# Kernel tuning notes

Hardware: AMD Instinct MI355X
Metric: run time of the kernel (lower is better)

Reference implementation:

```python
import jax, jax.numpy as jnp
import numpy as np

N_ATOMS = 5000
N_PAIRS = 160000
N_STRUCT = 16
N_SPECIES = 4
L_MAX = 2
K = 128            # k_max per l (rectangular)
N_BASIS = 8        # radial basis size
RAD_HIDDEN = 32    # radial MLP hidden
CUTOFF = 5.0
MSG_SCALE = 0.1767767   # ~1/sqrt(avg_degree)
INIT_SCALE = 0.2        # hypers['initial_scaling']


def _orthogonal(key, n):
    m = jax.random.normal(key, (n, n))
    q, r = jnp.linalg.qr(m)
    return q * jnp.sign(jnp.diag(r))[None, :]


def setup_inputs() -> dict:
    key = jax.random.key(0)
    ks = jax.random.split(key, 24)
    positions = jax.random.normal(ks[0], (N_ATOMS, 3)) * 1.5
    cells = jax.random.normal(ks[1], (N_STRUCT, 3, 3)) * 0.5
    species = jax.random.randint(ks[2], (N_ATOMS,), 0, N_SPECIES)
    cell_shifts = jax.random.randint(ks[3], (N_PAIRS, 3), 0, 3).astype(jnp.int32)
    center_indices = jax.random.randint(ks[4], (N_PAIRS,), 0, N_ATOMS)
    neighbor_indices = jax.random.randint(ks[5], (N_PAIRS,), 0, N_ATOMS)
    structure_pairs = jax.random.randint(ks[6], (N_PAIRS,), 0, N_STRUCT)
    s = lambda k, sh, f: jax.random.normal(k, sh) * f
    params = dict(
        embed=s(ks[7], (N_SPECIES, K), 1.0),
        rad_w1=s(ks[8], (N_BASIS, RAD_HIDDEN), 0.3), rad_b1=jnp.zeros((RAD_HIDDEN,)),
        rad_w2=s(ks[9], (RAD_HIDDEN, (L_MAX + 1) * K), 0.3), rad_b2=jnp.zeros(((L_MAX + 1) * K,)),
        erad_w1=s(ks[10], (N_BASIS, RAD_HIDDEN), 0.3), erad_b1=jnp.zeros((RAD_HIDDEN,)),
        erad_w2=s(ks[11], (RAD_HIDDEN, (L_MAX + 1) * K), 0.3), erad_b2=jnp.zeros(((L_MAX + 1) * K,)),
        mix_a=s(ks[12], (L_MAX + 1, K), 0.5),
        emix_a=s(ks[13], (L_MAX + 1, K), 0.5),
        head_w1=s(ks[14], (K, K), 0.1), head_b1=jnp.zeros((K,)),
        head_w2=s(ks[15], (K, K), 0.1), head_b2=jnp.zeros((K,)),
        last_w=s(ks[16], (K, 1), 0.1), last_b=jnp.zeros((1,)),
        U2=_orthogonal(ks[20], 9),  # orthogonal CG change-of-basis, U @ U.T = I
    )
    return dict(positions=positions, cells=cells, species=species,
                cell_shifts=cell_shifts, center_indices=center_indices,
                neighbor_indices=neighbor_indices, structure_pairs=structure_pairs,
                **params)


def _sph(unit):
    # real spherical harmonics up to l=2, inputs are unit vectors [P,3]
    x, y, z = unit[:, 0], unit[:, 1], unit[:, 2]
    sh0 = jnp.ones_like(x)[:, None]
    sh1 = jnp.stack([y, z, x], axis=1)
    c = jnp.sqrt(3.0)
    sh2 = jnp.stack([c * x * y, c * y * z, 0.5 * (3 * z * z - 1.0),
                     c * x * z, 0.5 * c * (x * x - y * y)], axis=1)
    return [sh0, sh1, sh2]


def _radial(d, w1, b1, w2, b2):
    # Gaussian radial basis * smooth cutoff -> MLP -> per-l K channels
    centers = jnp.linspace(0.0, CUTOFF, N_BASIS)
    rb = jnp.exp(-((d[:, None] - centers[None, :]) ** 2) / (2.0 * 0.5 ** 2))
    fcut = jnp.where(d < CUTOFF, 0.5 * (jnp.cos(jnp.pi * d / CUTOFF) + 1.0), 0.0)
    h = jax.nn.silu((rb * fcut[:, None]) @ w1 + b1)
    return (h @ w2 + b2).reshape(-1, L_MAX + 1, K)  # [P, l, K]


def _uncouple(f, l, U2):
    # coupled [N, 2l+1, K] -> uncoupled matrix [N, 3, 3, K] (padded_l = 2)
    if l == 0:
        return f[:, :, None, :]
    n, _, k = f.shape
    vec = jnp.zeros((n, 9, k), f.dtype)
    off = 1 if l == 1 else 4
    vec = vec.at[:, off:off + 2 * l + 1, :].set(f)
    unc = jnp.einsum('qp,nqk->npk', U2, vec)  # U2.T @ vec
    return unc.reshape(n, 3, 3, k)


def _couple(unc, l, U2):
    if l == 0:
        return unc[:, :, 0, :]
    n, k = unc.shape[0], unc.shape[-1]
    vec = jnp.einsum('pq,nqk->npk', U2, unc.reshape(n, 9, k))
    off = 1 if l == 1 else 4
    return vec[:, off:off + 2 * l + 1, :]


def _cg_iterate(feats, U2, mix):
    # CG tensor product iteration in the uncoupled (matrix) basis:
    # matrix product A@A is equivariant under A -> D A D^T
    out = []
    for l, f in enumerate(feats):
        A = _uncouple(f, l, U2)
        C = jnp.einsum('nimk,nmjk->nijk', A, A)
        out.append(_couple(A + C * mix[l][None, None, None, :], l, U2))
    return out


def _forward(positions, cells, embed, rad_w1, rad_b1, rad_w2, rad_b2,
             erad_w1, erad_b1, erad_w2, erad_b2, mix_a, emix_a,
             head_w1, head_b1, head_w2, head_b2, last_w, last_b, U2,
             species, cell_shifts, center_indices, neighbor_indices, structure_pairs):
    # pair vectors with PBC shifts
    shifts = cell_shifts.astype(positions.dtype) - 1.0  # -> {-1,0,1}
    vec = positions[neighbor_indices] - positions[center_indices] \
        + jnp.einsum('pi,pij->pj', shifts, cells[structure_pairs])
    d = jnp.sqrt(jnp.sum(vec * vec, axis=1) + 1e-12)
    unit = vec / d[:, None]
    sh = [s * INIT_SCALE for s in _sph(unit)]
    Rk = _radial(d, rad_w1, rad_b1, rad_w2, rad_b2)      # [P, 3, K]
    emb_n = embed[species][neighbor_indices]             # [P, K]

    # invariant message passing: sh_l x radial x neighbor embedding, scatter to centers
    feats = []
    for l in range(L_MAX + 1):
        msg = sh[l][:, :, None] * Rk[:, l, None, :] * emb_n[:, None, :]
        feats.append(jax.ops.segment_sum(msg, center_indices, num_segments=N_ATOMS) * MSG_SCALE)

    feats = _cg_iterate(feats, U2, mix_a)

    # equivariant message passing layer
    Rke = _radial(d, erad_w1, erad_b1, erad_w2, erad_b2)
    inv_n = feats[0][neighbor_indices, 0, :]             # [P, K] invariant part
    new = []
    for l in range(L_MAX + 1):
        g = feats[l][neighbor_indices]                   # [P, 2l+1, K]
        msg = sh[l][:, :, None] * Rke[:, l, None, :] * inv_n[:, None, :] \
            + Rke[:, 0, None, :] * g
        new.append(feats[l] + jax.ops.segment_sum(msg, center_indices, num_segments=N_ATOMS) * MSG_SCALE)

    feats = _cg_iterate(new, U2, emix_a)

    # scalar (l=0) MLP head + last linear layer
    h = feats[0][:, 0, :]
    h = jax.nn.silu(h @ head_w1 + head_b1)
    h = jax.nn.silu(h @ head_w2 + head_b2)
    return h @ last_w + last_b  # [N_ATOMS, 1]


def reference(positions, cells, species, cell_shifts, center_indices,
              neighbor_indices, structure_pairs, embed, rad_w1, rad_b1, rad_w2,
              rad_b2, erad_w1, erad_b1, erad_w2, erad_b2, mix_a, emix_a,
              head_w1, head_b1, head_w2, head_b2, last_w, last_b, U2):
    return _forward(positions, cells, embed, rad_w1, rad_b1, rad_w2, rad_b2,
                    erad_w1, erad_b1, erad_w2, erad_b2, mix_a, emix_a,
                    head_w1, head_b1, head_w2, head_b2, last_w, last_b, U2,
                    species, cell_shifts, center_indices, neighbor_indices,
                    structure_pairs)
```

## Files before the change

### kernel.cpp

```cpp
#include <hip/hip_runtime.h>

constexpr int   kAtoms  = 5000;
constexpr int   kPairs  = 160000;
constexpr int   KD      = 128;
constexpr int   NB      = 8;
constexpr int   RH      = 32;
constexpr float kCutoff = 5.0f;
constexpr float kPi     = 3.14159265358979323846f;
constexpr float C1 = 0.2f * 0.1767767f;
constexpr float C2 = 1.2f * 0.1767767f;
constexpr int   CHUNK = 96;

__device__ __forceinline__ float silu(float x) { return x / (1.0f + __expf(-x)); }


__global__ __launch_bounds__(256) void hist_kernel(
    const int* __restrict__ ctr, int* __restrict__ cnt)
{
    int p = blockIdx.x * 256 + threadIdx.x;
    atomicAdd(cnt + ctr[p], 1);
}

__global__ __launch_bounds__(1024) void scan_kernel(
    const int* __restrict__ cnt, int* __restrict__ off, int* __restrict__ cur)
{
    __shared__ int s_part[1024];
    const int CH = 5;
    int t = threadIdx.x;
    int base = t * CH;
    int loc[CH];
    int run = 0;
    #pragma unroll
    for (int i = 0; i < CH; i++) {
        int idx = base + i;
        int v = (idx < kAtoms) ? cnt[idx] : 0;
        loc[i] = run;
        run += v;
    }
    s_part[t] = run;
    __syncthreads();
    for (int st = 1; st < 1024; st <<= 1) {
        int v = (t >= st) ? s_part[t - st] : 0;
        __syncthreads();
        s_part[t] += v;
        __syncthreads();
    }
    int excl = (t > 0) ? s_part[t - 1] : 0;
    #pragma unroll
    for (int i = 0; i < CH; i++) {
        int idx = base + i;
        if (idx < kAtoms) { off[idx] = excl + loc[i]; cur[idx] = excl + loc[i]; }
    }
    if (t == 1023) off[kAtoms] = s_part[1023];
}

__global__ __launch_bounds__(256) void build_kernel(
    const float* __restrict__ pos, const float* __restrict__ cells,
    const int* __restrict__ species, const int* __restrict__ shifts,
    const int* __restrict__ ctr, const int* __restrict__ nbr,
    const int* __restrict__ spair,
    int* __restrict__ cur, int* __restrict__ nbrs_s, int* __restrict__ specs_s,
    float* __restrict__ rbf_s)
{
    int p = blockIdx.x * 256 + threadIdx.x;
    int ci = ctr[p], ni = nbr[p], sp = spair[p];
    float s0 = (float)shifts[p * 3 + 0] - 1.0f;
    float s1 = (float)shifts[p * 3 + 1] - 1.0f;
    float s2 = (float)shifts[p * 3 + 2] - 1.0f;
    const float* C = cells + sp * 9;
    float vx = pos[ni * 3 + 0] - pos[ci * 3 + 0] + s0 * C[0] + s1 * C[3] + s2 * C[6];
    float vy = pos[ni * 3 + 1] - pos[ci * 3 + 1] + s0 * C[1] + s1 * C[4] + s2 * C[7];
    float vz = pos[ni * 3 + 2] - pos[ci * 3 + 2] + s0 * C[2] + s1 * C[5] + s2 * C[8];
    float d = sqrtf(vx * vx + vy * vy + vz * vz + 1e-12f);
    float fcut = (d < kCutoff) ? 0.5f * (__cosf(kPi * d / kCutoff) + 1.0f) : 0.0f;

    int slot = atomicAdd(cur + ci, 1);
    nbrs_s[slot]  = ni;
    specs_s[slot] = species[ni];

    float r[NB];
    #pragma unroll
    for (int i = 0; i < NB; i++) {
        float tt = d - (kCutoff / (NB - 1)) * (float)i;
        r[i] = __expf(-2.0f * tt * tt) * fcut;
    }
    float4* dst = (float4*)(rbf_s + (size_t)slot * NB);
    dst[0] = make_float4(r[0], r[1], r[2], r[3]);
    dst[1] = make_float4(r[4], r[5], r[6], r[7]);
}

__global__ __launch_bounds__(64) void f0_kernel(
    const float* __restrict__ rbf_s, const int* __restrict__ specs_s,
    const int* __restrict__ off,
    const float* __restrict__ embed,
    const float* __restrict__ w1, const float* __restrict__ b1,
    const float* __restrict__ w2, const float* __restrict__ b2,
    const float* __restrict__ mix,
    float* __restrict__ G0)
{
    __shared__ float s_w1[NB][RH];
    __shared__ float s_b1v[RH];
    __shared__ float s_Hp[2][4][RH];
    __shared__ float s_H[4][RH];
    __shared__ float s_np[2][4];
    __shared__ float s_nc[4];

    int t = threadIdx.x;
    for (int idx = t; idx < NB * RH; idx += 64)
        s_w1[idx >> 5][idx & 31] = w1[idx];
    if (t < RH) s_b1v[t] = b1[t];
    __syncthreads();

    int a = blockIdx.x;
    int start = off[a], m = off[a + 1] - start;

    int g = t >> 5, j = t & 31;
    float H0 = 0, H1 = 0, H2 = 0, H3 = 0;
    int   n0 = 0, n1 = 0, n2 = 0, n3 = 0;
    float b1j = s_b1v[j];
    for (int pr = g; pr < m; pr += 2) {
        const float* rb = rbf_s + (size_t)(start + pr) * NB;
        float acc = b1j;
        #pragma unroll
        for (int i = 0; i < NB; i++) acc += rb[i] * s_w1[i][j];
        float h = silu(acc);
        int s = specs_s[start + pr];
        H0 += (s == 0) ? h : 0.0f;  H1 += (s == 1) ? h : 0.0f;
        H2 += (s == 2) ? h : 0.0f;  H3 += (s == 3) ? h : 0.0f;
        n0 += (s == 0); n1 += (s == 1); n2 += (s == 2); n3 += (s == 3);
    }
    s_Hp[g][0][j] = H0; s_Hp[g][1][j] = H1;
    s_Hp[g][2][j] = H2; s_Hp[g][3][j] = H3;
    if (j == 0) {
        s_np[g][0] = (float)n0; s_np[g][1] = (float)n1;
        s_np[g][2] = (float)n2; s_np[g][3] = (float)n3;
    }
    __syncthreads();
    for (int e = t; e < 4 * RH; e += 64) {
        int s = e >> 5, jj = e & 31;
        s_H[s][jj] = s_Hp[0][s][jj] + s_Hp[1][s][jj];
    }
    if (t < 4) s_nc[t] = s_np[0][t] + s_np[1][t];
    __syncthreads();

    float nc0 = s_nc[0], nc1 = s_nc[1], nc2 = s_nc[2], nc3 = s_nc[3];
    #pragma unroll
    for (int half = 0; half < 2; half++) {
        int k = t + 64 * half;
        float e0 = embed[0 * KD + k], e1 = embed[1 * KD + k];
        float e2 = embed[2 * KD + k], e3 = embed[3 * KD + k];
        float P0 = 0, P1 = 0, P2 = 0, P3 = 0;
        #pragma unroll 2
        for (int jq = 0; jq < RH / 4; jq++) {
            float4 h0 = *(const float4*)&s_H[0][4 * jq];
            float4 h1 = *(const float4*)&s_H[1][4 * jq];
            float4 h2 = *(const float4*)&s_H[2][4 * jq];
            float4 h3 = *(const float4*)&s_H[3][4 * jq];
            float wa = w2[(4 * jq + 0) * (3 * KD) + k];
            float wb = w2[(4 * jq + 1) * (3 * KD) + k];
            float wc = w2[(4 * jq + 2) * (3 * KD) + k];
            float wd = w2[(4 * jq + 3) * (3 * KD) + k];
            P0 += h0.x * wa + h0.y * wb + h0.z * wc + h0.w * wd;
            P1 += h1.x * wa + h1.y * wb + h1.z * wc + h1.w * wd;
            P2 += h2.x * wa + h2.y * wb + h2.z * wc + h2.w * wd;
            P3 += h3.x * wa + h3.y * wb + h3.z * wc + h3.w * wd;
        }
        float F = b2[k] * (nc0 * e0 + nc1 * e1 + nc2 * e2 + nc3 * e3)
                + e0 * P0 + e1 * P1 + e2 * P2 + e3 * P3;
        float F0v = C1 * F;
        G0[(size_t)a * KD + k] = F0v + F0v * F0v * mix[k];
    }
}

__global__ __launch_bounds__(64) void d0_kernel(
    const float* __restrict__ rbf_s, const int* __restrict__ nbrs_s,
    const int* __restrict__ off,
    const float* __restrict__ w1, const float* __restrict__ b1,
    const float* __restrict__ w2, const float* __restrict__ b2,
    const float* __restrict__ emix,
    const float* __restrict__ G0,
    float* __restrict__ V)
{
    __shared__ float s_w1[NB][RH];
    __shared__ float s_b1v[RH];
    __shared__ float s_h[CHUNK][RH];
    __shared__ int   s_nbr[CHUNK];

    int t = threadIdx.x;
    for (int idx = t; idx < NB * RH; idx += 64)
        s_w1[idx >> 5][idx & 31] = w1[idx];
    if (t < RH) s_b1v[t] = b1[t];

    int a = blockIdx.x;
    int start = off[a], end = off[a + 1];
    int k0 = t, k1 = t + 64;

    float w2c0[RH], w2c1[RH];
    #pragma unroll
    for (int j = 0; j < RH; j++) {
        w2c0[j] = w2[j * (3 * KD) + k0];
        w2c1[j] = w2[j * (3 * KD) + k1];
    }
    float b2k0 = b2[k0], b2k1 = b2[k1];

    int g = t >> 5, j = t & 31;
    float b1j = s_b1v[j];

    float Dacc0 = 0.0f, Dacc1 = 0.0f;
    for (int c = start; c < end; c += CHUNK) {
        int m = min(CHUNK, end - c);
        __syncthreads();
        for (int pr = g; pr < m; pr += 2) {
            const float* rb = rbf_s + (size_t)(c + pr) * NB;
            float acc = b1j;
            #pragma unroll
            for (int i = 0; i < NB; i++) acc += rb[i] * s_w1[i][j];
            s_h[pr][j] = silu(acc);
        }
        for (int i = t; i < m; i += 64) s_nbr[i] = nbrs_s[c + i];
        __syncthreads();
        for (int i = 0; i < m; i++) {
            const float* gbase = G0 + (size_t)s_nbr[i] * KD;
            float gv0 = gbase[k0];
            float gv1 = gbase[k1];
            float R0 = b2k0, R1 = b2k1;
            #pragma unroll
            for (int jq = 0; jq < RH / 4; jq++) {
                float4 h4 = *(const float4*)&s_h[i][4 * jq];
                R0 += h4.x * w2c0[4 * jq + 0] + h4.y * w2c0[4 * jq + 1]
                    + h4.z * w2c0[4 * jq + 2] + h4.w * w2c0[4 * jq + 3];
                R1 += h4.x * w2c1[4 * jq + 0] + h4.y * w2c1[4 * jq + 1]
                    + h4.z * w2c1[4 * jq + 2] + h4.w * w2c1[4 * jq + 3];
            }
            Dacc0 += R0 * gv0;
            Dacc1 += R1 * gv1;
        }
    }
    float n0 = G0[(size_t)a * KD + k0] + C2 * Dacc0;
    float n1 = G0[(size_t)a * KD + k1] + C2 * Dacc1;
    V[(size_t)a * KD + k0] = n0 + n0 * n0 * emix[k0];
    V[(size_t)a * KD + k1] = n1 + n1 * n1 * emix[k1];
}

__global__ __launch_bounds__(128) void head_kernel(
    const float* __restrict__ V,
    const float* __restrict__ w1, const float* __restrict__ b1,
    const float* __restrict__ w2, const float* __restrict__ b2,
    const float* __restrict__ lw, const float* __restrict__ lb,
    float* __restrict__ out)
{
    __shared__ float s_a[8][KD];
    __shared__ float s_b[8][KD];
    int j = threadIdx.x;
    int abase = blockIdx.x * 8;

    #pragma unroll
    for (int a = 0; a < 8; a++) {
        int ga = abase + a;
        s_a[a][j] = (ga < kAtoms) ? V[(size_t)ga * KD + j] : 0.0f;
    }
    __syncthreads();

    float acc[8];
    float bj = b1[j];
    #pragma unroll
    for (int a = 0; a < 8; a++) acc[a] = bj;
    for (int kk = 0; kk < KD; kk += 4) {
        float wa = w1[(kk + 0) * KD + j], wb = w1[(kk + 1) * KD + j];
        float wc = w1[(kk + 2) * KD + j], wd = w1[(kk + 3) * KD + j];
        #pragma unroll
        for (int a = 0; a < 8; a++) {
            float4 v = *(const float4*)&s_a[a][kk];
            acc[a] += v.x * wa + v.y * wb + v.z * wc + v.w * wd;
        }
    }
    #pragma unroll
    for (int a = 0; a < 8; a++) s_b[a][j] = silu(acc[a]);
    __syncthreads();

    float b2j = b2[j];
    #pragma unroll
    for (int a = 0; a < 8; a++) acc[a] = b2j;
    for (int kk = 0; kk < KD; kk += 4) {
        float wa = w2[(kk + 0) * KD + j], wb = w2[(kk + 1) * KD + j];
        float wc = w2[(kk + 2) * KD + j], wd = w2[(kk + 3) * KD + j];
        #pragma unroll
        for (int a = 0; a < 8; a++) {
            float4 v = *(const float4*)&s_b[a][kk];
            acc[a] += v.x * wa + v.y * wb + v.z * wc + v.w * wd;
        }
    }
    float lwj = lw[j];
    __syncthreads();
    #pragma unroll
    for (int a = 0; a < 8; a++) s_a[a][j] = silu(acc[a]) * lwj;
    __syncthreads();
    for (int s = 64; s > 0; s >>= 1) {
        if (j < s) {
            #pragma unroll
            for (int a = 0; a < 8; a++) s_a[a][j] += s_a[a][j + s];
        }
        __syncthreads();
    }
    if (j < 8) {
        int ga = abase + j;
        if (ga < kAtoms) out[ga] = s_a[j][0] + lb[0];
    }
}

extern "C" void kernel_launch(void* const* d_in, const int* in_sizes, int n_in,
                              void* d_out, int out_size, void* d_ws, size_t ws_size,
                              hipStream_t stream) {
    const float* positions = (const float*)d_in[0];
    const float* cells     = (const float*)d_in[1];
    const int*   species   = (const int*)d_in[2];
    const int*   shifts    = (const int*)d_in[3];
    const int*   ctr       = (const int*)d_in[4];
    const int*   nbr       = (const int*)d_in[5];
    const int*   spair     = (const int*)d_in[6];
    const float* embed     = (const float*)d_in[7];
    const float* rad_w1    = (const float*)d_in[8];
    const float* rad_b1    = (const float*)d_in[9];
    const float* rad_w2    = (const float*)d_in[10];
    const float* rad_b2    = (const float*)d_in[11];
    const float* erad_w1   = (const float*)d_in[12];
    const float* erad_b1   = (const float*)d_in[13];
    const float* erad_w2   = (const float*)d_in[14];
    const float* erad_b2   = (const float*)d_in[15];
    const float* mix_a     = (const float*)d_in[16];
    const float* emix_a    = (const float*)d_in[17];
    const float* head_w1   = (const float*)d_in[18];
    const float* head_b1   = (const float*)d_in[19];
    const float* head_w2   = (const float*)d_in[20];
    const float* head_b2   = (const float*)d_in[21];
    const float* last_w    = (const float*)d_in[22];
    const float* last_b    = (const float*)d_in[23];

    float* rbf_s = (float*)d_ws;
    float* G0    = rbf_s + (size_t)kPairs * NB;
    float* V     = G0    + (size_t)kAtoms * KD;
    int*   cnt   = (int*)(V + (size_t)kAtoms * KD);
    int*   off   = cnt + kAtoms;
    int*   cur   = off + kAtoms + 1;
    int*   nbrs  = cur + kAtoms;
    int*   specs = nbrs + kPairs;

    hipMemsetAsync(cnt, 0, kAtoms * sizeof(int), stream);

    hist_kernel<<<kPairs / 256, 256, 0, stream>>>(ctr, cnt);
    scan_kernel<<<1, 1024, 0, stream>>>(cnt, off, cur);
    build_kernel<<<kPairs / 256, 256, 0, stream>>>(
        positions, cells, species, shifts, ctr, nbr, spair,
        cur, nbrs, specs, rbf_s);

    f0_kernel<<<kAtoms, 64, 0, stream>>>(
        rbf_s, specs, off, embed, rad_w1, rad_b1, rad_w2, rad_b2,
        mix_a, G0);

    d0_kernel<<<kAtoms, 64, 0, stream>>>(
        rbf_s, nbrs, off, erad_w1, erad_b1, erad_w2, erad_b2,
        emix_a, G0, V);

    head_kernel<<<(kAtoms + 7) / 8, 128, 0, stream>>>(
        V, head_w1, head_b1, head_w2, head_b2, last_w, last_b,
        (float*)d_out);
}
```

Measured before the change: 220.1 us.

## Retile f0/d0 kernels: two atoms per f0 block, one channel per d0 thread

The f0 kernel now packs two atoms into a 128-thread block, each handled by its own 64-thread half with separate shared buffers. The d0 kernel moves to 128 threads, one output channel per thread, which halves the register-resident w2 columns and allows higher occupancy. The neighbor chunk shrinks to 32, and the next neighbor's G0 value is prefetched inside the loop. The cost is more blocks' worth of weight loads and rbf MLP work per chunk, plus an extra sync in d0.

```diff
diff --git a/kernel.cpp b/kernel.cpp
--- a/kernel.cpp
+++ b/kernel.cpp
@@ -9,7 +9,7 @@
 constexpr float kPi     = 3.14159265358979323846f;
 constexpr float C1 = 0.2f * 0.1767767f;
 constexpr float C2 = 1.2f * 0.1767767f;
-constexpr int   CHUNK = 96;
+constexpr int   CHUNK = 32;
 
 __device__ __forceinline__ float silu(float x) { return x / (1.0f + __expf(-x)); }
 
@@ -89,7 +89,7 @@
     dst[1] = make_float4(r[4], r[5], r[6], r[7]);
 }
 
-__global__ __launch_bounds__(64) void f0_kernel(
+__global__ __launch_bounds__(128) void f0_kernel(
     const float* __restrict__ rbf_s, const int* __restrict__ specs_s,
     const int* __restrict__ off,
     const float* __restrict__ embed,
@@ -100,21 +100,23 @@
 {
     __shared__ float s_w1[NB][RH];
     __shared__ float s_b1v[RH];
-    __shared__ float s_Hp[2][4][RH];
-    __shared__ float s_H[4][RH];
-    __shared__ float s_np[2][4];
-    __shared__ float s_nc[4];
+    __shared__ float s_Hp[2][2][4][RH];
+    __shared__ float s_H[2][4][RH];
+    __shared__ float s_np[2][2][4];
+    __shared__ float s_nc[2][4];
 
     int t = threadIdx.x;
-    for (int idx = t; idx < NB * RH; idx += 64)
+    int w = t >> 6;
+    int t64 = t & 63;
+    for (int idx = t; idx < NB * RH; idx += 128)
         s_w1[idx >> 5][idx & 31] = w1[idx];
     if (t < RH) s_b1v[t] = b1[t];
     __syncthreads();
 
-    int a = blockIdx.x;
+    int a = blockIdx.x * 2 + w;
     int start = off[a], m = off[a + 1] - start;
 
-    int g = t >> 5, j = t & 31;
+    int g = t64 >> 5, j = t64 & 31;
     float H0 = 0, H1 = 0, H2 = 0, H3 = 0;
     int   n0 = 0, n1 = 0, n2 = 0, n3 = 0;
     float b1j = s_b1v[j];
@@ -129,33 +131,33 @@
         H2 += (s == 2) ? h : 0.0f;  H3 += (s == 3) ? h : 0.0f;
         n0 += (s == 0); n1 += (s == 1); n2 += (s == 2); n3 += (s == 3);
     }
-    s_Hp[g][0][j] = H0; s_Hp[g][1][j] = H1;
-    s_Hp[g][2][j] = H2; s_Hp[g][3][j] = H3;
+    s_Hp[w][g][0][j] = H0; s_Hp[w][g][1][j] = H1;
+    s_Hp[w][g][2][j] = H2; s_Hp[w][g][3][j] = H3;
     if (j == 0) {
-        s_np[g][0] = (float)n0; s_np[g][1] = (float)n1;
-        s_np[g][2] = (float)n2; s_np[g][3] = (float)n3;
-    }
-    __syncthreads();
-    for (int e = t; e < 4 * RH; e += 64) {
+        s_np[w][g][0] = (float)n0; s_np[w][g][1] = (float)n1;
+        s_np[w][g][2] = (float)n2; s_np[w][g][3] = (float)n3;
+    }
+    __syncthreads();
+    for (int e = t64; e < 4 * RH; e += 64) {
         int s = e >> 5, jj = e & 31;
-        s_H[s][jj] = s_Hp[0][s][jj] + s_Hp[1][s][jj];
-    }
-    if (t < 4) s_nc[t] = s_np[0][t] + s_np[1][t];
-    __syncthreads();
-
-    float nc0 = s_nc[0], nc1 = s_nc[1], nc2 = s_nc[2], nc3 = s_nc[3];
+        s_H[w][s][jj] = s_Hp[w][0][s][jj] + s_Hp[w][1][s][jj];
+    }
+    if (t64 < 4) s_nc[w][t64] = s_np[w][0][t64] + s_np[w][1][t64];
+    __syncthreads();
+
+    float nc0 = s_nc[w][0], nc1 = s_nc[w][1], nc2 = s_nc[w][2], nc3 = s_nc[w][3];
     #pragma unroll
     for (int half = 0; half < 2; half++) {
-        int k = t + 64 * half;
+        int k = t64 + 64 * half;
         float e0 = embed[0 * KD + k], e1 = embed[1 * KD + k];
         float e2 = embed[2 * KD + k], e3 = embed[3 * KD + k];
         float P0 = 0, P1 = 0, P2 = 0, P3 = 0;
         #pragma unroll 2
         for (int jq = 0; jq < RH / 4; jq++) {
-            float4 h0 = *(const float4*)&s_H[0][4 * jq];
-            float4 h1 = *(const float4*)&s_H[1][4 * jq];
-            float4 h2 = *(const float4*)&s_H[2][4 * jq];
-            float4 h3 = *(const float4*)&s_H[3][4 * jq];
+            float4 h0 = *(const float4*)&s_H[w][0][4 * jq];
+            float4 h1 = *(const float4*)&s_H[w][1][4 * jq];
+            float4 h2 = *(const float4*)&s_H[w][2][4 * jq];
+            float4 h3 = *(const float4*)&s_H[w][3][4 * jq];
             float wa = w2[(4 * jq + 0) * (3 * KD) + k];
             float wb = w2[(4 * jq + 1) * (3 * KD) + k];
             float wc = w2[(4 * jq + 2) * (3 * KD) + k];
@@ -172,7 +174,7 @@
     }
 }
 
-__global__ __launch_bounds__(64) void d0_kernel(
+__global__ __launch_bounds__(128, 8) void d0_kernel(
     const float* __restrict__ rbf_s, const int* __restrict__ nbrs_s,
     const int* __restrict__ off,
     const float* __restrict__ w1, const float* __restrict__ b1,
@@ -187,59 +189,53 @@
     __shared__ int   s_nbr[CHUNK];
 
     int t = threadIdx.x;
-    for (int idx = t; idx < NB * RH; idx += 64)
+    for (int idx = t; idx < NB * RH; idx += 128)
         s_w1[idx >> 5][idx & 31] = w1[idx];
     if (t < RH) s_b1v[t] = b1[t];
+    __syncthreads();
 
     int a = blockIdx.x;
     int start = off[a], end = off[a + 1];
-    int k0 = t, k1 = t + 64;
-
-    float w2c0[RH], w2c1[RH];
-    #pragma unroll
-    for (int j = 0; j < RH; j++) {
-        w2c0[j] = w2[j * (3 * KD) + k0];
-        w2c1[j] = w2[j * (3 * KD) + k1];
-    }
-    float b2k0 = b2[k0], b2k1 = b2[k1];
+    int k = t;
+
+    float w2c[RH];
+    #pragma unroll
+    for (int j = 0; j < RH; j++) w2c[j] = w2[j * (3 * KD) + k];
+    float b2k = b2[k];
 
     int g = t >> 5, j = t & 31;
     float b1j = s_b1v[j];
 
-    float Dacc0 = 0.0f, Dacc1 = 0.0f;
+    float Dacc = 0.0f;
     for (int c = start; c < end; c += CHUNK) {
         int m = min(CHUNK, end - c);
         __syncthreads();
-        for (int pr = g; pr < m; pr += 2) {
+        for (int pr = g; pr < m; pr += 4) {
             const float* rb = rbf_s + (size_t)(c + pr) * NB;
             float acc = b1j;
             #pragma unroll
             for (int i = 0; i < NB; i++) acc += rb[i] * s_w1[i][j];
             s_h[pr][j] = silu(acc);
         }
-        for (int i = t; i < m; i += 64) s_nbr[i] = nbrs_s[c + i];
-        __syncthreads();
+        for (int i = t; i < m; i += 128) s_nbr[i] = nbrs_s[c + i];
+        __syncthreads();
+
+        float gv_next = G0[(size_t)s_nbr[0] * KD + k];
         for (int i = 0; i < m; i++) {
-            const float* gbase = G0 + (size_t)s_nbr[i] * KD;
-            float gv0 = gbase[k0];
-            float gv1 = gbase[k1];
-            float R0 = b2k0, R1 = b2k1;
+            float gv = gv_next;
+            if (i + 1 < m) gv_next = G0[(size_t)s_nbr[i + 1] * KD + k];
+            float R = b2k;
             #pragma unroll
             for (int jq = 0; jq < RH / 4; jq++) {
                 float4 h4 = *(const float4*)&s_h[i][4 * jq];
-                R0 += h4.x * w2c0[4 * jq + 0] + h4.y * w2c0[4 * jq + 1]
-                    + h4.z * w2c0[4 * jq + 2] + h4.w * w2c0[4 * jq + 3];
-                R1 += h4.x * w2c1[4 * jq + 0] + h4.y * w2c1[4 * jq + 1]
-                    + h4.z * w2c1[4 * jq + 2] + h4.w * w2c1[4 * jq + 3];
+                R += h4.x * w2c[4 * jq + 0] + h4.y * w2c[4 * jq + 1]
+                   + h4.z * w2c[4 * jq + 2] + h4.w * w2c[4 * jq + 3];
             }
-            Dacc0 += R0 * gv0;
-            Dacc1 += R1 * gv1;
-        }
-    }
-    float n0 = G0[(size_t)a * KD + k0] + C2 * Dacc0;
-    float n1 = G0[(size_t)a * KD + k1] + C2 * Dacc1;
-    V[(size_t)a * KD + k0] = n0 + n0 * n0 * emix[k0];
-    V[(size_t)a * KD + k1] = n1 + n1 * n1 * emix[k1];
+            Dacc += R * gv;
+        }
+    }
+    float n0 = G0[(size_t)a * KD + k] + C2 * Dacc;
+    V[(size_t)a * KD + k] = n0 + n0 * n0 * emix[k];
 }
 
 __global__ __launch_bounds__(128) void head_kernel(
@@ -353,11 +349,11 @@
         positions, cells, species, shifts, ctr, nbr, spair,
         cur, nbrs, specs, rbf_s);
 
-    f0_kernel<<<kAtoms, 64, 0, stream>>>(
+    f0_kernel<<<kAtoms / 2, 128, 0, stream>>>(
         rbf_s, specs, off, embed, rad_w1, rad_b1, rad_w2, rad_b2,
         mix_a, G0);
 
-    d0_kernel<<<kAtoms, 64, 0, stream>>>(
+    d0_kernel<<<kAtoms, 128, 0, stream>>>(
         rbf_s, nbrs, off, erad_w1, erad_b1, erad_w2, erad_b2,
         emix_a, G0, V);
 
```

New measurement: 284.8 us. 1.29x slower.

## Replace CSR sort-by-center with atomic scatter aggregation in pair order

Applied to the files above, without the earlier changes.

Removes the histogram/scan/bucket build and processes pairs in their original order. Per-(atom,species) hidden sums are now accumulated with global float atomics in the build kernel, and the message sum D is scattered with atomics from a grid-strided pair kernel. The final nonlinearity moves into the head kernel. In exchange it adds heavy atomic traffic (32 atomics per pair into H, and 128 per pair into D) and makes float summation order nondeterministic.

```diff
diff --git a/kernel.cpp b/kernel.cpp
--- a/kernel.cpp
+++ b/kernel.cpp
@@ -9,60 +9,30 @@
 constexpr float kPi     = 3.14159265358979323846f;
 constexpr float C1 = 0.2f * 0.1767767f;
 constexpr float C2 = 1.2f * 0.1767767f;
-constexpr int   CHUNK = 96;
 
 __device__ __forceinline__ float silu(float x) { return x / (1.0f + __expf(-x)); }
 
 
-__global__ __launch_bounds__(256) void hist_kernel(
-    const int* __restrict__ ctr, int* __restrict__ cnt)
-{
-    int p = blockIdx.x * 256 + threadIdx.x;
-    atomicAdd(cnt + ctr[p], 1);
-}
-
-__global__ __launch_bounds__(1024) void scan_kernel(
-    const int* __restrict__ cnt, int* __restrict__ off, int* __restrict__ cur)
-{
-    __shared__ int s_part[1024];
-    const int CH = 5;
-    int t = threadIdx.x;
-    int base = t * CH;
-    int loc[CH];
-    int run = 0;
-    #pragma unroll
-    for (int i = 0; i < CH; i++) {
-        int idx = base + i;
-        int v = (idx < kAtoms) ? cnt[idx] : 0;
-        loc[i] = run;
-        run += v;
-    }
-    s_part[t] = run;
-    __syncthreads();
-    for (int st = 1; st < 1024; st <<= 1) {
-        int v = (t >= st) ? s_part[t - st] : 0;
-        __syncthreads();
-        s_part[t] += v;
-        __syncthreads();
-    }
-    int excl = (t > 0) ? s_part[t - 1] : 0;
-    #pragma unroll
-    for (int i = 0; i < CH; i++) {
-        int idx = base + i;
-        if (idx < kAtoms) { off[idx] = excl + loc[i]; cur[idx] = excl + loc[i]; }
-    }
-    if (t == 1023) off[kAtoms] = s_part[1023];
-}
-
-__global__ __launch_bounds__(256) void build_kernel(
+__global__ __launch_bounds__(256) void build2_kernel(
     const float* __restrict__ pos, const float* __restrict__ cells,
     const int* __restrict__ species, const int* __restrict__ shifts,
     const int* __restrict__ ctr, const int* __restrict__ nbr,
     const int* __restrict__ spair,
-    int* __restrict__ cur, int* __restrict__ nbrs_s, int* __restrict__ specs_s,
-    float* __restrict__ rbf_s)
+    const float* __restrict__ w1, const float* __restrict__ b1,
+    float* __restrict__ rbf_s, float* __restrict__ H, int* __restrict__ ncnt)
 {
-    int p = blockIdx.x * 256 + threadIdx.x;
+    __shared__ float s_w1[NB][RH];
+    __shared__ float s_b1v[RH];
+    __shared__ float s_rbf[256][NB];
+    __shared__ int   s_ci[256];
+    __shared__ int   s_sp[256];
+
+    int t = threadIdx.x;
+    for (int idx = t; idx < NB * RH; idx += 256)
+        s_w1[idx >> 5][idx & 31] = w1[idx];
+    if (t < RH) s_b1v[t] = b1[t];
+
+    int p  = blockIdx.x * 256 + t;
     int ci = ctr[p], ni = nbr[p], sp = spair[p];
     float s0 = (float)shifts[p * 3 + 0] - 1.0f;
     float s1 = (float)shifts[p * 3 + 1] - 1.0f;
@@ -74,176 +44,148 @@
     float d = sqrtf(vx * vx + vy * vy + vz * vz + 1e-12f);
     float fcut = (d < kCutoff) ? 0.5f * (__cosf(kPi * d / kCutoff) + 1.0f) : 0.0f;
 
-    int slot = atomicAdd(cur + ci, 1);
-    nbrs_s[slot]  = ni;
-    specs_s[slot] = species[ni];
-
     float r[NB];
     #pragma unroll
     for (int i = 0; i < NB; i++) {
         float tt = d - (kCutoff / (NB - 1)) * (float)i;
         r[i] = __expf(-2.0f * tt * tt) * fcut;
     }
-    float4* dst = (float4*)(rbf_s + (size_t)slot * NB);
-    dst[0] = make_float4(r[0], r[1], r[2], r[3]);
-    dst[1] = make_float4(r[4], r[5], r[6], r[7]);
-}
-
-__global__ __launch_bounds__(64) void f0_kernel(
-    const float* __restrict__ rbf_s, const int* __restrict__ specs_s,
-    const int* __restrict__ off,
+    float4 r0 = make_float4(r[0], r[1], r[2], r[3]);
+    float4 r1 = make_float4(r[4], r[5], r[6], r[7]);
+    float4* dst = (float4*)(rbf_s + (size_t)p * NB);
+    dst[0] = r0; dst[1] = r1;
+    *(float4*)&s_rbf[t][0] = r0;
+    *(float4*)&s_rbf[t][4] = r1;
+    int spec = species[ni];
+    s_ci[t] = ci; s_sp[t] = spec;
+    atomicAdd(&ncnt[ci * 4 + spec], 1);
+    __syncthreads();
+
+    int wv = t >> 6, lane = t & 63, hh = lane >> 5, j = lane & 31;
+    float b1j = s_b1v[j];
+    for (int q = 0; q < 32; q++) {
+        int idx = wv * 64 + 2 * q + hh;
+        float acc = b1j;
+        #pragma unroll
+        for (int i = 0; i < NB; i++) acc += s_rbf[idx][i] * s_w1[i][j];
+        float h = silu(acc);
+        int a = s_ci[idx], s = s_sp[idx];
+        atomicAdd(&H[(size_t)(a * 4 + s) * RH + j], h);
+    }
+}
+
+__global__ __launch_bounds__(256) void f0b_kernel(
+    const float* __restrict__ H, const int* __restrict__ ncnt,
     const float* __restrict__ embed,
-    const float* __restrict__ w1, const float* __restrict__ b1,
     const float* __restrict__ w2, const float* __restrict__ b2,
     const float* __restrict__ mix,
     float* __restrict__ G0)
 {
-    __shared__ float s_w1[NB][RH];
-    __shared__ float s_b1v[RH];
-    __shared__ float s_Hp[2][4][RH];
-    __shared__ float s_H[4][RH];
-    __shared__ float s_np[2][4];
-    __shared__ float s_nc[4];
-
-    int t = threadIdx.x;
-    for (int idx = t; idx < NB * RH; idx += 64)
-        s_w1[idx >> 5][idx & 31] = w1[idx];
-    if (t < RH) s_b1v[t] = b1[t];
-    __syncthreads();
-
-    int a = blockIdx.x;
-    int start = off[a], m = off[a + 1] - start;
-
-    int g = t >> 5, j = t & 31;
-    float H0 = 0, H1 = 0, H2 = 0, H3 = 0;
-    int   n0 = 0, n1 = 0, n2 = 0, n3 = 0;
-    float b1j = s_b1v[j];
-    for (int pr = g; pr < m; pr += 2) {
-        const float* rb = rbf_s + (size_t)(start + pr) * NB;
-        float acc = b1j;
-        #pragma unroll
-        for (int i = 0; i < NB; i++) acc += rb[i] * s_w1[i][j];
-        float h = silu(acc);
-        int s = specs_s[start + pr];
-        H0 += (s == 0) ? h : 0.0f;  H1 += (s == 1) ? h : 0.0f;
-        H2 += (s == 2) ? h : 0.0f;  H3 += (s == 3) ? h : 0.0f;
-        n0 += (s == 0); n1 += (s == 1); n2 += (s == 2); n3 += (s == 3);
-    }
-    s_Hp[g][0][j] = H0; s_Hp[g][1][j] = H1;
-    s_Hp[g][2][j] = H2; s_Hp[g][3][j] = H3;
-    if (j == 0) {
-        s_np[g][0] = (float)n0; s_np[g][1] = (float)n1;
-        s_np[g][2] = (float)n2; s_np[g][3] = (float)n3;
-    }
-    __syncthreads();
-    for (int e = t; e < 4 * RH; e += 64) {
-        int s = e >> 5, jj = e & 31;
-        s_H[s][jj] = s_Hp[0][s][jj] + s_Hp[1][s][jj];
-    }
-    if (t < 4) s_nc[t] = s_np[0][t] + s_np[1][t];
-    __syncthreads();
-
-    float nc0 = s_nc[0], nc1 = s_nc[1], nc2 = s_nc[2], nc3 = s_nc[3];
-    #pragma unroll
-    for (int half = 0; half < 2; half++) {
-        int k = t + 64 * half;
-        float e0 = embed[0 * KD + k], e1 = embed[1 * KD + k];
-        float e2 = embed[2 * KD + k], e3 = embed[3 * KD + k];
-        float P0 = 0, P1 = 0, P2 = 0, P3 = 0;
-        #pragma unroll 2
-        for (int jq = 0; jq < RH / 4; jq++) {
-            float4 h0 = *(const float4*)&s_H[0][4 * jq];
-            float4 h1 = *(const float4*)&s_H[1][4 * jq];
-            float4 h2 = *(const float4*)&s_H[2][4 * jq];
-            float4 h3 = *(const float4*)&s_H[3][4 * jq];
-            float wa = w2[(4 * jq + 0) * (3 * KD) + k];
-            float wb = w2[(4 * jq + 1) * (3 * KD) + k];
-            float wc = w2[(4 * jq + 2) * (3 * KD) + k];
-            float wd = w2[(4 * jq + 3) * (3 * KD) + k];
-            P0 += h0.x * wa + h0.y * wb + h0.z * wc + h0.w * wd;
-            P1 += h1.x * wa + h1.y * wb + h1.z * wc + h1.w * wd;
-            P2 += h2.x * wa + h2.y * wb + h2.z * wc + h2.w * wd;
-            P3 += h3.x * wa + h3.y * wb + h3.z * wc + h3.w * wd;
-        }
-        float F = b2[k] * (nc0 * e0 + nc1 * e1 + nc2 * e2 + nc3 * e3)
-                + e0 * P0 + e1 * P1 + e2 * P2 + e3 * P3;
-        float F0v = C1 * F;
-        G0[(size_t)a * KD + k] = F0v + F0v * F0v * mix[k];
-    }
-}
-
-__global__ __launch_bounds__(64) void d0_kernel(
-    const float* __restrict__ rbf_s, const int* __restrict__ nbrs_s,
-    const int* __restrict__ off,
-    const float* __restrict__ w1, const float* __restrict__ b1,
-    const float* __restrict__ w2, const float* __restrict__ b2,
-    const float* __restrict__ emix,
-    const float* __restrict__ G0,
-    float* __restrict__ V)
+    __shared__ float s_H[2][4 * RH];
+    __shared__ float s_n[2][4];
+    int t  = threadIdx.x;
+    int at = t >> 7;
+    int k  = t & 127;
+    int a  = blockIdx.x * 2 + at;
+    s_H[at][k] = H[(size_t)a * 128 + k];
+    if (k < 4) s_n[at][k] = (float)ncnt[a * 4 + k];
+    __syncthreads();
+
+    float e0 = embed[0 * KD + k], e1 = embed[1 * KD + k];
+    float e2 = embed[2 * KD + k], e3 = embed[3 * KD + k];
+    float F2 = 0.0f;
+    #pragma unroll 4
+    for (int j = 0; j < RH; j++) {
+        float tj = e0 * s_H[at][0 * RH + j] + e1 * s_H[at][1 * RH + j]
+                 + e2 * s_H[at][2 * RH + j] + e3 * s_H[at][3 * RH + j];
+        F2 += w2[j * (3 * KD) + k] * tj;
+    }
+    float F = b2[k] * (s_n[at][0] * e0 + s_n[at][1] * e1
+                     + s_n[at][2] * e2 + s_n[at][3] * e3) + F2;
+    float F0v = C1 * F;
+    G0[(size_t)a * KD + k] = F0v + F0v * F0v * mix[k];
+}
+
+__global__ __launch_bounds__(256, 2) void d0b_kernel(
+    const float* __restrict__ rbf_s,
+    const int* __restrict__ ctr, const int* __restrict__ nbr,
+    const float* __restrict__ w1e, const float* __restrict__ b1e,
+    const float* __restrict__ w2e, const float* __restrict__ b2e,
+    const float* __restrict__ G0, float* __restrict__ D)
 {
     __shared__ float s_w1[NB][RH];
     __shared__ float s_b1v[RH];
-    __shared__ float s_h[CHUNK][RH];
-    __shared__ int   s_nbr[CHUNK];
+    __shared__ float s_rbf[64][NB];
+    __shared__ float s_h[64][RH];
+    __shared__ int   s_ci[64];
+    __shared__ int   s_nbr[64];
 
     int t = threadIdx.x;
-    for (int idx = t; idx < NB * RH; idx += 64)
-        s_w1[idx >> 5][idx & 31] = w1[idx];
-    if (t < RH) s_b1v[t] = b1[t];
-
-    int a = blockIdx.x;
-    int start = off[a], end = off[a + 1];
-    int k0 = t, k1 = t + 64;
-
+    for (int idx = t; idx < NB * RH; idx += 256)
+        s_w1[idx >> 5][idx & 31] = w1e[idx];
+    if (t < RH) s_b1v[t] = b1e[t];
+
+    int wv = t >> 6, lane = t & 63;
+    int k0 = lane, k1 = lane + 64;
     float w2c0[RH], w2c1[RH];
     #pragma unroll
     for (int j = 0; j < RH; j++) {
-        w2c0[j] = w2[j * (3 * KD) + k0];
-        w2c1[j] = w2[j * (3 * KD) + k1];
-    }
-    float b2k0 = b2[k0], b2k1 = b2[k1];
-
-    int g = t >> 5, j = t & 31;
-    float b1j = s_b1v[j];
-
-    float Dacc0 = 0.0f, Dacc1 = 0.0f;
-    for (int c = start; c < end; c += CHUNK) {
-        int m = min(CHUNK, end - c);
+        w2c0[j] = w2e[j * (3 * KD) + k0];
+        w2c1[j] = w2e[j * (3 * KD) + k1];
+    }
+    float b2k0 = b2e[k0], b2k1 = b2e[k1];
+    __syncthreads();
+    float b1j = s_b1v[t & 31];
+
+    const int NBATCH = kPairs / 64;
+    for (int b = blockIdx.x; b < NBATCH; b += gridDim.x) {
+        int base = b * 64;
+        if (t < 128)
+            *(float4*)&s_rbf[t >> 1][(t & 1) * 4] =
+                *(const float4*)(rbf_s + (size_t)(base + (t >> 1)) * NB + (t & 1) * 4);
+        if (t < 64) { s_ci[t] = ctr[base + t]; s_nbr[t] = nbr[base + t]; }
         __syncthreads();
-        for (int pr = g; pr < m; pr += 2) {
-            const float* rb = rbf_s + (size_t)(c + pr) * NB;
-            float acc = b1j;
-            #pragma unroll
-            for (int i = 0; i < NB; i++) acc += rb[i] * s_w1[i][j];
-            s_h[pr][j] = silu(acc);
-        }
-        for (int i = t; i < m; i += 64) s_nbr[i] = nbrs_s[c + i];
+        {
+            int j = t & 31;
+            for (int pp = t >> 5; pp < 64; pp += 8) {
+                float acc = b1j;
+                #pragma unroll
+                for (int i = 0; i < NB; i++) acc += s_rbf[pp][i] * s_w1[i][j];
+                s_h[pp][j] = silu(acc);
+            }
+        }
         __syncthreads();
-        for (int i = 0; i < m; i++) {
-            const float* gbase = G0 + (size_t)s_nbr[i] * KD;
-            float gv0 = gbase[k0];
-            float gv1 = gbase[k1];
+        int pbase = wv * 16;
+        int nb0 = s_nbr[pbase];
+        float gv0n = G0[(size_t)nb0 * KD + k0];
+        float gv1n = G0[(size_t)nb0 * KD + k1];
+        for (int i = 0; i < 16; i++) {
+            float gv0 = gv0n, gv1 = gv1n;
+            if (i + 1 < 16) {
+                int nbn = s_nbr[pbase + i + 1];
+                gv0n = G0[(size_t)nbn * KD + k0];
+                gv1n = G0[(size_t)nbn * KD + k1];
+            }
             float R0 = b2k0, R1 = b2k1;
             #pragma unroll
             for (int jq = 0; jq < RH / 4; jq++) {
-                float4 h4 = *(const float4*)&s_h[i][4 * jq];
+                float4 h4 = *(const float4*)&s_h[pbase + i][4 * jq];
                 R0 += h4.x * w2c0[4 * jq + 0] + h4.y * w2c0[4 * jq + 1]
                     + h4.z * w2c0[4 * jq + 2] + h4.w * w2c0[4 * jq + 3];
                 R1 += h4.x * w2c1[4 * jq + 0] + h4.y * w2c1[4 * jq + 1]
                     + h4.z * w2c1[4 * jq + 2] + h4.w * w2c1[4 * jq + 3];
             }
-            Dacc0 += R0 * gv0;
-            Dacc1 += R1 * gv1;
-        }
-    }
-    float n0 = G0[(size_t)a * KD + k0] + C2 * Dacc0;
-    float n1 = G0[(size_t)a * KD + k1] + C2 * Dacc1;
-    V[(size_t)a * KD + k0] = n0 + n0 * n0 * emix[k0];
-    V[(size_t)a * KD + k1] = n1 + n1 * n1 * emix[k1];
+            int ci = s_ci[pbase + i];
+            atomicAdd(&D[(size_t)ci * KD + k0], R0 * gv0);
+            atomicAdd(&D[(size_t)ci * KD + k1], R1 * gv1);
+        }
+        __syncthreads();
+    }
 }
 
 __global__ __launch_bounds__(128) void head_kernel(
-    const float* __restrict__ V,
+    const float* __restrict__ G0, const float* __restrict__ D,
+    const float* __restrict__ emix,
     const float* __restrict__ w1, const float* __restrict__ b1,
     const float* __restrict__ w2, const float* __restrict__ b2,
     const float* __restrict__ lw, const float* __restrict__ lb,
@@ -253,11 +195,15 @@
     __shared__ float s_b[8][KD];
     int j = threadIdx.x;
     int abase = blockIdx.x * 8;
+    float emj = emix[j];
 
     #pragma unroll
     for (int a = 0; a < 8; a++) {
         int ga = abase + a;
-        s_a[a][j] = (ga < kAtoms) ? V[(size_t)ga * KD + j] : 0.0f;
+        float g  = G0[(size_t)ga * KD + j];
+        float dd = D[(size_t)ga * KD + j];
+        float n0 = g + C2 * dd;
+        s_a[a][j] = n0 + n0 * n0 * emj;
     }
     __syncthreads();
 
@@ -336,32 +282,28 @@
     const float* last_w    = (const float*)d_in[22];
     const float* last_b    = (const float*)d_in[23];
 
-    float* rbf_s = (float*)d_ws;
-    float* G0    = rbf_s + (size_t)kPairs * NB;
-    float* V     = G0    + (size_t)kAtoms * KD;
-    int*   cnt   = (int*)(V + (size_t)kAtoms * KD);
-    int*   off   = cnt + kAtoms;
-    int*   cur   = off + kAtoms + 1;
-    int*   nbrs  = cur + kAtoms;
-    int*   specs = nbrs + kPairs;
-
-    hipMemsetAsync(cnt, 0, kAtoms * sizeof(int), stream);
-
-    hist_kernel<<<kPairs / 256, 256, 0, stream>>>(ctr, cnt);
-    scan_kernel<<<1, 1024, 0, stream>>>(cnt, off, cur);
-    build_kernel<<<kPairs / 256, 256, 0, stream>>>(
+    float* H     = (float*)d_ws;
+    int*   ncnt  = (int*)(H + (size_t)kAtoms * KD);
+    float* D     = (float*)(ncnt + (size_t)kAtoms * 4);
+    float* G0    = D + (size_t)kAtoms * KD;
+    float* rbf_s = G0 + (size_t)kAtoms * KD;
+
+    size_t zero_bytes = (size_t)kAtoms * KD * 4
+                      + (size_t)kAtoms * 4 * 4
+                      + (size_t)kAtoms * KD * 4;
+    hipMemsetAsync(d_ws, 0, zero_bytes, stream);
+
+    build2_kernel<<<kPairs / 256, 256, 0, stream>>>(
         positions, cells, species, shifts, ctr, nbr, spair,
-        cur, nbrs, specs, rbf_s);
-
-    f0_kernel<<<kAtoms, 64, 0, stream>>>(
-        rbf_s, specs, off, embed, rad_w1, rad_b1, rad_w2, rad_b2,
-        mix_a, G0);
-
-    d0_kernel<<<kAtoms, 64, 0, stream>>>(
-        rbf_s, nbrs, off, erad_w1, erad_b1, erad_w2, erad_b2,
-        emix_a, G0, V);
-
-    head_kernel<<<(kAtoms + 7) / 8, 128, 0, stream>>>(
-        V, head_w1, head_b1, head_w2, head_b2, last_w, last_b,
+        rad_w1, rad_b1, rbf_s, H, ncnt);
+
+    f0b_kernel<<<kAtoms / 2, 256, 0, stream>>>(
+        H, ncnt, embed, rad_w2, rad_b2, mix_a, G0);
+
+    d0b_kernel<<<1250, 256, 0, stream>>>(
+        rbf_s, ctr, nbr, erad_w1, erad_b1, erad_w2, erad_b2, G0, D);
+
+    head_kernel<<<kAtoms / 8, 128, 0, stream>>>(
+        G0, D, emix_a, head_w1, head_b1, head_w2, head_b2, last_w, last_b,
         (float*)d_out);
 }
```

Result: slower. 243.9 us (+10.9%).
